# Kernel tuning notes

Measured on AMD Instinct MI355X. Metric: run time of the kernel, lower is better.

The kernel has to match this reference:

```python
import jax, jax.numpy as jnp
import numpy as np

B, N, F, S = 32, 512, 101, 10   # batch, set size, str_fea_len, expansion_size
E, H, L = 128, 4, 3             # embed_dim, num_heads, n_encoders
EH = E * H
TAB = 100                       # atom-feature table rows


def _ln(x, g, b, eps=1e-5):
    m = jnp.mean(x, -1, keepdims=True)
    v = jnp.var(x, -1, keepdims=True)
    return (x - m) / jnp.sqrt(v + eps) * g + b


def setup_inputs() -> dict:
    key = jax.random.key(0)
    ks = iter(jax.random.split(key, 48))
    nrm = lambda shape: jax.random.normal(next(ks), shape, jnp.float32) * 0.05
    return {
        'str_fea': jax.random.uniform(next(ks), (B, N, F), jnp.float32),
        'comp_fea': jax.random.randint(next(ks), (B, N), 0, TAB),
        'cell_fea': jax.random.normal(next(ks), (B, 6), jnp.float32),
        'af_table': jax.random.uniform(next(ks), (TAB, 92), jnp.float32),
        'comp_w': nrm((92, E)), 'comp_b': jnp.zeros((E,), jnp.float32),
        'emb_w': nrm(((F - 1) * S, E)), 'emb_b': jnp.zeros((E,), jnp.float32),
        'ln_g': jnp.ones((L, E), jnp.float32), 'ln_b': jnp.zeros((L, E), jnp.float32),
        'wq': nrm((L, E, EH)), 'bq': jnp.zeros((L, EH), jnp.float32),
        'wk': nrm((L, E, EH)), 'bk': jnp.zeros((L, EH), jnp.float32),
        'wv': nrm((L, E, EH)), 'bv': jnp.zeros((L, EH), jnp.float32),
        'inproj_w': nrm((L, EH, 3 * EH)), 'inproj_b': jnp.zeros((L, 3 * EH), jnp.float32),
        'out_w': nrm((L, EH, E)), 'out_b': jnp.zeros((L, E), jnp.float32),
        'ffn_w': nrm((L, E, E)), 'ffn_b': jnp.zeros((L, E), jnp.float32),
        'ln2_g': jnp.ones((E,), jnp.float32), 'ln2_b': jnp.zeros((E,), jnp.float32),
        'final_w': nrm((E, 1)), 'final_b': jnp.zeros((1,), jnp.float32),
    }


def reference(str_fea, comp_fea, cell_fea, af_table, comp_w, comp_b, emb_w, emb_b,
              ln_g, ln_b, wq, bq, wk, bk, wv, bv, inproj_w, inproj_b,
              out_w, out_b, ffn_w, ffn_b, ln2_g, ln2_b, final_w, final_b):
    weights = str_fea[:, :, 0:1]                                  # [B,N,1]
    # AtomFeaturizer + composition embedding
    comp = af_table[comp_fea] @ comp_w + comp_b                   # [B,N,E]
    # DistanceExpansion: (1 - (d - i/S))**2 for i in 0..S-1
    d = str_fea[:, :, 1:]                                         # [B,N,F-1]
    starter = jnp.arange(S, dtype=str_fea.dtype) / S
    de = (1.0 - (d[..., None] - starter)) ** 2                    # [B,N,F-1,S]
    de = de.reshape(d.shape[0], d.shape[1], (F - 1) * S)
    strf = de @ emb_w + emb_b                                     # [B,N,E]
    x = comp + strf
    x_init = x
    mask = jnp.sum(weights, -1) == 0.0                            # [B,N] key padding
    w_row = weights[..., 0]                                       # [B,N]
    hd = EH // H
    scale = 1.0 / np.sqrt(hd)
    for l in range(L):
        xn = _ln(x, ln_g[l], ln_b[l])
        qin = xn @ wq[l] + bq[l]                                  # [B,N,EH]
        kin = xn @ wk[l] + bk[l]
        vin = xn @ wv[l] + bv[l]                                  # used as V in manual attention
        # torch.nn.MultiheadAttention in-projection (v-block unused: att_output discarded)
        q = qin @ inproj_w[l][:, :EH] + inproj_b[l][:EH]
        k = kin @ inproj_w[l][:, EH:2 * EH] + inproj_b[l][EH:2 * EH]
        qh = q.reshape(q.shape[0], q.shape[1], H, hd)
        kh = k.reshape(k.shape[0], k.shape[1], H, hd)
        logits = jnp.einsum('bihd,bjhd->bhij', qh, kh) * scale    # [B,H,N,N]
        logits = jnp.where(mask[:, None, None, :], -1e9, logits)
        attn = jnp.mean(jax.nn.softmax(logits, -1), axis=1)       # head-averaged [B,N,N]
        # external edge-weight masking + renormalization
        aw = attn * w_row[:, None, :]
        aw = aw / jnp.sum(aw, -1, keepdims=True)
        att_out = jnp.einsum('bij,bjd->bid', aw, vin)             # [B,N,EH]
        o1 = x + att_out @ out_w[l] + out_b[l]
        o2 = jax.nn.softplus(_ln(o1, ln_g[l], ln_b[l]) @ ffn_w[l] + ffn_b[l])
        x = _ln(o1 + o2, ln_g[l], ln_b[l])
    x = jnp.sum(weights * (x + x_init), axis=1)                   # weighted pool [B,E]
    x = _ln(x, ln2_g, ln2_b)
    return x @ final_w + final_b                                  # [B,1]
```

## Files before the change

### kernel.cpp

```cpp
#include <hip/hip_runtime.h>
#include <math.h>

#define B_ 32
#define N_ 512
#define F_ 101
#define E_ 128
#define H_ 4
#define EH_ 512
#define L_ 3
#define M_ (B_*N_)

typedef __attribute__((ext_vector_type(8))) short s8v;
typedef __attribute__((ext_vector_type(8))) unsigned short us8v;
typedef __attribute__((ext_vector_type(4))) float f4v;
typedef __attribute__((ext_vector_type(4))) unsigned int u4v;

__device__ __forceinline__ unsigned short f2bf(float f){
  unsigned int u = __builtin_bit_cast(unsigned int, f);
  u += 0x7fffu + ((u>>16)&1u);
  return (unsigned short)(u>>16);
}
__device__ __forceinline__ float bf2f(unsigned int h){
  unsigned int u = h<<16; return __builtin_bit_cast(float, u);
}
__device__ __forceinline__ float softplus_f(float v) {
  return fmaxf(v, 0.f) + log1pf(__expf(-fabsf(v)));
}

#define GLOAD16(gp, lp) __builtin_amdgcn_global_load_lds( \
    (__attribute__((address_space(1))) unsigned int*)(gp), \
    (__attribute__((address_space(3))) unsigned int*)(lp), 16, 0, 0)

#define MFMA16(a,b,c) __builtin_amdgcn_mfma_f32_16x16x32_bf16(a,b,c,0,0,0)

__global__ __launch_bounds__(256) void prepA_kernel(
    const float* __restrict__ wq, const float* __restrict__ wk,
    const float* __restrict__ bq, const float* __restrict__ bk,
    const float* __restrict__ inproj_w,
    float* __restrict__ effpart, float* __restrict__ bpart) {
  __shared__ float As[64][132];
  __shared__ float Bs[64][68];
  const int blk = blockIdx.x;
  const int t = threadIdx.x;
  if (blk < 384) {
    const int bx = blk % 48, ks = blk / 48;
    const int lq = bx>>3, nt = bx&7;
    const int l = lq>>1, qk = lq&1;
    const int bn = nt*64;
    const int k0 = ks*64;
    const float* A = (qk ? wk : wq) + (size_t)l*128*512;
    const float* IP = inproj_w + (size_t)l*512*1536 + qk*512 + bn;
    float acc[8][4];
    #pragma unroll
    for (int i=0;i<8;++i)
      #pragma unroll
      for (int j=0;j<4;++j) acc[i][j]=0.f;
    const int r0 = (t&15)*8, c0 = (t>>4)*4;
    {
      int r = t & 127, half = t>>7;
      #pragma unroll
      for (int u=0;u<8;++u){
        float4 a = *(const float4*)(A + (size_t)r*512 + k0 + half*32 + u*4);
        int kk = half*32 + u*4;
        As[kk+0][r]=a.x; As[kk+1][r]=a.y; As[kk+2][r]=a.z; As[kk+3][r]=a.w;
      }
      int kk = t>>2, cb = (t&3)*16;
      #pragma unroll
      for (int u=0;u<4;++u)
        *(float4*)&Bs[kk][cb+u*4] = *(const float4*)(IP + (size_t)(k0+kk)*1536 + cb + u*4);
    }
    __syncthreads();
    for (int k2=0;k2<64;++k2){
      float4 b = *(const float4*)&Bs[k2][c0];
      float4 a0 = *(const float4*)&As[k2][r0];
      float4 a1 = *(const float4*)&As[k2][r0+4];
      float av[8] = {a0.x,a0.y,a0.z,a0.w,a1.x,a1.y,a1.z,a1.w};
      #pragma unroll
      for (int i=0;i<8;++i){
        acc[i][0] += av[i]*b.x; acc[i][1] += av[i]*b.y;
        acc[i][2] += av[i]*b.z; acc[i][3] += av[i]*b.w;
      }
    }
    #pragma unroll
    for (int j=0;j<4;++j){
      float* dst = effpart + (((size_t)ks*48 + bx)*64 + c0 + j)*128 + r0;
      float4 v0 = {acc[0][j], acc[1][j], acc[2][j], acc[3][j]};
      float4 v1 = {acc[4][j], acc[5][j], acc[6][j], acc[7][j]};
      *(float4*)dst = v0;
      *(float4*)(dst+4) = v1;
    }
  } else {
    const int idxb = blk - 384;
    const int lq = idxb>>3, kt = idxb&7;
    const int l = lq>>1, qk = lq&1;
    const float* bv = (qk?bk:bq) + l*512 + kt*64;
    const float* IP = inproj_w + ((size_t)l*512 + kt*64)*1536 + qk*512;
    float a0=0.f, a1=0.f;
    for (int kk=0; kk<64; ++kk){
      float b = bv[kk];
      const float* row = IP + (size_t)kk*1536;
      a0 += b*row[t];
      a1 += b*row[t+256];
    }
    bpart[(lq*8+kt)*512 + t]       = a0;
    bpart[(lq*8+kt)*512 + t + 256] = a1;
  }
}

__global__ __launch_bounds__(256) void prepB_kernel(
    const float* __restrict__ effpart, const float* __restrict__ bpart,
    const float* __restrict__ wv, const float* __restrict__ out_w,
    const float* __restrict__ ffn_w,
    const float* __restrict__ inproj_b, const float* __restrict__ bvv,
    const float* __restrict__ emb_w, const float* __restrict__ comp_w,
    const float* __restrict__ str_fea, const int* __restrict__ comp_fea,
    const float* __restrict__ af_table,
    unsigned short* __restrict__ wqkvT, unsigned short* __restrict__ outT,
    unsigned short* __restrict__ ffnT, float* __restrict__ bqkv,
    unsigned short* __restrict__ WHi, unsigned short* __restrict__ WLo,
    float* __restrict__ Cpart,
    unsigned short* __restrict__ FHi, unsigned short* __restrict__ FLo,
    float* __restrict__ w_row) {
  const int blk = blockIdx.x;
  const int t = threadIdx.x;
  if (blk < 1536) {
    int idx = blk*256 + t;
    int m = idx & 127;
    int n = (idx>>7) & 511;
    int lq = idx >> 16;
    int l = lq>>1, qk = lq&1;
    size_t base = (((size_t)(lq*8 + (n>>6)))*64 + (n&63))*128 + m;
    float v = 0.f;
    #pragma unroll
    for (int ks=0;ks<8;++ks) v += effpart[(size_t)ks*393216 + base];
    wqkvT[((size_t)l*1536 + qk*512 + n)*128 + m] = f2bf(v);
  } else if (blk < 1662) {
    const int b2 = blk - 1536;
    if (b2 < 108) {
      __shared__ float tile[64][65];
      const float* src; unsigned short* dst; int srcld, dstld;
      if (b2 < 48) {
        int lay = b2/16, rem = b2%16, kt = rem>>3, nt = rem&7;
        src = wv + ((size_t)lay*128 + kt*64)*512 + nt*64; srcld = 512;
        dst = wqkvT + ((size_t)lay*1536 + 1024 + nt*64)*128 + kt*64; dstld = 128;
      } else if (b2 < 96) {
        int b3 = b2-48; int lay = b3/16, rem = b3%16, kt = rem>>1, nt = rem&1;
        src = out_w + ((size_t)lay*512 + kt*64)*128 + nt*64; srcld = 128;
        dst = outT + ((size_t)lay*128 + nt*64)*512 + kt*64; dstld = 512;
      } else {
        int b4 = b2-96; int lay = b4/4, rem = b4%4, kt = rem>>1, nt = rem&1;
        src = ffn_w + ((size_t)lay*128 + kt*64)*128 + nt*64; srcld = 128;
        dst = ffnT + ((size_t)lay*128 + nt*64)*128 + kt*64; dstld = 128;
      }
      #pragma unroll
      for (int rp=0; rp<4; ++rp){
        int r = rp*16 + (t>>4), c = (t&15)*4;
        float4 v = *(const float4*)(src + (size_t)r*srcld + c);
        tile[r][c+0]=v.x; tile[r][c+1]=v.y; tile[r][c+2]=v.z; tile[r][c+3]=v.w;
      }
      __syncthreads();
      #pragma unroll
      for (int wp=0; wp<2; ++wp){
        int n = wp*32 + (t>>3), kk = (t&7)*8;
        us8v pk;
        #pragma unroll
        for (int e=0;e<8;++e) pk[e] = f2bf(tile[kk+e][n]);
        *(us8v*)(dst + (size_t)n*dstld + kk) = pk;
      }
    } else {
      int idx = (b2-108)*256 + t;
      if (idx < 4608) {
        int l = idx/1536, n = idx - l*1536;
        float v;
        if (n < 1024) {
          int qk = n>>9, c = n&511;
          v = inproj_b[(size_t)l*1536 + n];
          #pragma unroll
          for (int kt=0;kt<8;++kt) v += bpart[((l*2+qk)*8+kt)*512 + c];
        } else {
          v = bvv[(size_t)l*512 + (n-1024)];
        }
        bqkv[idx] = v;
      }
    }
  } else if (blk < 1674) {
    if (t < 128) {
      int p = blk - 1662, e = t;
      if (p < 10) {
        float Cp = 0.f;
        for (int ff=0; ff<10; ++ff){
          int f = p*10+ff;
          float A=0.f, Bv=0.f;
          #pragma unroll
          for (int s=0;s<10;++s){
            float wvv = emb_w[(size_t)(f*10+s)*128 + e];
            A += wvv; Bv += 0.2f*s*wvv; Cp += 0.01f*(s*s)*wvv;
          }
          int kA = 92+f, kB = 192+f;
          unsigned short hA = f2bf(A);
          WHi[e*320+kA]=hA; WLo[e*320+kA]=f2bf(A - bf2f(hA));
          unsigned short hB = f2bf(Bv);
          WHi[e*320+kB]=hB; WLo[e*320+kB]=f2bf(Bv - bf2f(hB));
        }
        Cpart[p*128+e] = Cp;
      } else if (p == 10) {
        for (int kk=0;kk<92;++kk){
          float v = comp_w[(size_t)kk*128 + e];
          unsigned short h = f2bf(v);
          WHi[e*320+kk]=h; WLo[e*320+kk]=f2bf(v - bf2f(h));
        }
      } else {
        for (int kk=292;kk<320;++kk){ WHi[e*320+kk]=0; WLo[e*320+kk]=0; }
      }
    }
  } else {
    int g = (blk-1674)*256 + t;
    int row = g / 40, seg = g - row*40;
    const float* sr = str_fea + (size_t)row*F_;
    if (seg == 0) w_row[row] = sr[0];
    const float* af = af_table + (size_t)comp_fea[row]*92;
    const int c0 = seg*8;
    us8v hi, lo;
    #pragma unroll
    for (int e=0;e<8;++e){
      int kk = c0+e; float v;
      if (kk < 92) v = af[kk];
      else if (kk < 192) { float u = 1.f - sr[1+kk-92]; v = u*u; }
      else if (kk < 292) v = 1.f - sr[1+kk-192];
      else v = 0.f;
      unsigned short h = f2bf(v);
      hi[e] = h; lo[e] = f2bf(v - bf2f(h));
    }
    *(us8v*)(FHi + (size_t)row*320 + c0) = hi;
    *(us8v*)(FLo + (size_t)row*320 + c0) = lo;
  }
}

__global__ __launch_bounds__(256) void embgemm_kernel(
    const unsigned short* __restrict__ FHi, const unsigned short* __restrict__ FLo,
    const unsigned short* __restrict__ WHi, const unsigned short* __restrict__ WLo,
    const float* __restrict__ Cpart, const float* __restrict__ comp_b,
    const float* __restrict__ emb_b,
    const float* __restrict__ g0, const float* __restrict__ b0,
    float* __restrict__ x, float* __restrict__ x_init,
    unsigned short* __restrict__ xnb) {
  __shared__ unsigned short lds[24576];
  unsigned short* AHi = lds;
  unsigned short* ALo = lds + 4096;
  unsigned short* BHi = lds + 8192;
  unsigned short* BLo = lds + 16384;
  const int bm = blockIdx.x*64;
  const int t = threadIdx.x, w = t>>6, l = t&63;
  f4v acc[8];
  #pragma unroll
  for (int i=0;i<8;++i) acc[i] = (f4v){0.f,0.f,0.f,0.f};
  const int srow = t>>3, sseg = t&7;
  for (int k0=0;k0<320;k0+=64){
    #pragma unroll
    for (int c=0;c<2;++c){
      int row = c*32+srow;
      GLOAD16(FHi + (size_t)(bm+row)*320 + k0 + ((sseg^(row&7))<<3), (char*)AHi + c*4096 + w*1024);
      GLOAD16(FLo + (size_t)(bm+row)*320 + k0 + ((sseg^(row&7))<<3), (char*)ALo + c*4096 + w*1024);
    }
    #pragma unroll
    for (int c=0;c<4;++c){
      int row = c*32+srow;
      GLOAD16(WHi + (size_t)row*320 + k0 + ((sseg^(row&7))<<3), (char*)BHi + c*4096 + w*1024);
      GLOAD16(WLo + (size_t)row*320 + k0 + ((sseg^(row&7))<<3), (char*)BLo + c*4096 + w*1024);
    }
    __syncthreads();
    #pragma unroll
    for (int ks=0;ks<2;++ks){
      int arow = w*16 + (l&15);
      int aswz = ((((l>>4)+ks*4) ^ (arow&7))<<4);
      s8v ah = *(const s8v*)((const char*)AHi + arow*128 + aswz);
      s8v al = *(const s8v*)((const char*)ALo + arow*128 + aswz);
      #pragma unroll
      for (int ct=0;ct<8;++ct){
        int col = ct*16 + (l&15);
        int bswz = ((((l>>4)+ks*4) ^ (col&7))<<4);
        s8v bh = *(const s8v*)((const char*)BHi + col*128 + bswz);
        s8v bl = *(const s8v*)((const char*)BLo + col*128 + bswz);
        acc[ct] = MFMA16(ah, bh, acc[ct]);
        acc[ct] = MFMA16(ah, bl, acc[ct]);
        acc[ct] = MFMA16(al, bh, acc[ct]);
      }
    }
    __syncthreads();
  }
  float vv[8][4], gc[8], bc[8];
  #pragma unroll
  for (int ct=0;ct<8;++ct){
    int c = ct*16 + (l&15);
    float be = comp_b[c] + emb_b[c];
    for (int p=0;p<10;++p) be += Cpart[p*128+c];
    gc[ct] = g0[c]; bc[ct] = b0[c];
    #pragma unroll
    for (int r=0;r<4;++r) vv[ct][r] = acc[ct][r] + be;
  }
  #pragma unroll
  for (int r=0;r<4;++r){
    float s=0.f, sq=0.f;
    #pragma unroll
    for (int ct=0;ct<8;++ct){ s += vv[ct][r]; sq += vv[ct][r]*vv[ct][r]; }
    #pragma unroll
    for (int m=1;m<16;m<<=1){ s += __shfl_xor(s,m,64); sq += __shfl_xor(sq,m,64); }
    float mean = s*(1.f/128.f);
    float rstd = rsqrtf(sq*(1.f/128.f) - mean*mean + 1e-5f);
    int row = bm + w*16 + (l>>4)*4 + r;
    #pragma unroll
    for (int ct=0;ct<8;++ct){
      int c = ct*16 + (l&15);
      float v = vv[ct][r];
      x[(size_t)row*128 + c] = v;
      x_init[(size_t)row*128 + c] = v;
      xnb[(size_t)row*128 + c] = f2bf((v-mean)*rstd*gc[ct] + bc[ct]);
    }
  }
}

template<int RT>
__global__ __launch_bounds__(256) void mgemm_kernel(
    const unsigned short* __restrict__ A,
    const unsigned short* __restrict__ Bt,
    const float* __restrict__ bias,
    unsigned short* __restrict__ Cb,
    unsigned short* __restrict__ vT,
    int K) {
  constexpr int BM = RT*32;
  __shared__ float smem[8192];
  unsigned short* Al = (unsigned short*)smem;
  unsigned short* Bl = Al + BM*64;
  const int bm = blockIdx.x*BM;
  const int bn = blockIdx.y*128;
  const int t = threadIdx.x;
  const int w = t>>6, l = t&63;
  const int wr = w>>1, wc = w&1;
  f4v acc[RT][4];
  #pragma unroll
  for (int i=0;i<RT;++i)
    #pragma unroll
    for (int j=0;j<4;++j) acc[i][j] = (f4v){0.f,0.f,0.f,0.f};
  const int srow = t>>3, sseg = t&7;
  for (int k0 = 0; k0 < K; k0 += 64) {
    #pragma unroll
    for (int c=0;c<BM/32;++c){
      int row = c*32 + srow;
      GLOAD16(A + (size_t)(bm+row)*K + k0 + ((sseg ^ (row&7))<<3),
              (char*)Al + c*4096 + w*1024);
    }
    #pragma unroll
    for (int c=0;c<4;++c){
      int row = c*32 + srow;
      GLOAD16(Bt + (size_t)(bn+row)*K + k0 + ((sseg ^ (row&7))<<3),
              (char*)Bl + c*4096 + w*1024);
    }
    __syncthreads();
    #pragma unroll
    for (int ks=0;ks<2;++ks){
      s8v bf[4];
      #pragma unroll
      for (int ct=0;ct<4;++ct){
        int col = wc*64 + ct*16 + (l&15);
        bf[ct] = *(const s8v*)((const char*)Bl + col*128 + ((((l>>4)+ks*4) ^ (col&7))<<4));
      }
      #pragma unroll
      for (int rt=0;rt<RT;++rt){
        int arow = wr*(RT*16) + rt*16 + (l&15);
        s8v af = *(const s8v*)((const char*)Al + arow*128 + ((((l>>4)+ks*4) ^ (arow&7))<<4));
        #pragma unroll
        for (int ct=0;ct<4;++ct)
          acc[rt][ct] = MFMA16(af, bf[ct], acc[rt][ct]);
      }
    }
    __syncthreads();
  }
  float bia[4];
  #pragma unroll
  for (int ct=0;ct<4;++ct) bia[ct] = bias[bn + wc*64 + ct*16 + (l&15)];
  unsigned short* lds16 = (unsigned short*)smem;
  if (bn < 1024) {
    #pragma unroll
    for (int rt=0;rt<RT;++rt)
      #pragma unroll
      for (int ct=0;ct<4;++ct)
        #pragma unroll
        for (int r=0;r<4;++r){
          int rr = wr*(RT*16) + rt*16 + (l>>4)*4 + r;
          int cc = wc*64 + ct*16 + (l&15);
          lds16[rr*128 + cc] = f2bf(acc[rt][ct][r] + bia[ct]);
        }
    __syncthreads();
    #pragma unroll
    for (int it=0; it<BM/16; ++it){
      int row = it*16 + (t>>4), seg = t&15;
      u4v v = *(const u4v*)(lds16 + row*128 + seg*8);
      *(u4v*)(Cb + (size_t)(bm+row)*1024 + bn + seg*8) = v;
    }
  } else {
    #pragma unroll
    for (int rt=0;rt<RT;++rt)
      #pragma unroll
      for (int ct=0;ct<4;++ct){
        int rbase = bm + wr*(RT*16) + rt*16 + (l>>4)*4;
        int bb = rbase >> 9, nn = rbase & 511;
        int d = bn - 1024 + wc*64 + ct*16 + (l&15);
        unsigned int lo = (unsigned int)f2bf(acc[rt][ct][0] + bia[ct])
                        | ((unsigned int)f2bf(acc[rt][ct][1] + bia[ct])<<16);
        unsigned int hi = (unsigned int)f2bf(acc[rt][ct][2] + bia[ct])
                        | ((unsigned int)f2bf(acc[rt][ct][3] + bia[ct])<<16);
        uint2 pk; pk.x = lo; pk.y = hi;
        *(uint2*)(vT + ((size_t)(bb*512 + d))*512 + nn) = pk;
      }
  }
}

#define STG_KH(dst, hh, j0s) { \
  _Pragma("unroll") \
  for (int c_=0;c_<8;++c_){ \
    int row_ = c_*32 + w*4 + (l>>4); \
    GLOAD16(qkb + (size_t)(b*512 + (j0s) + row_)*1024 + 512 + (hh)*128 + (((l&15) ^ (row_&7))<<3), \
            (dst) + c_*8192 + w*1024); } }

#define STG_VT(dst, j0s) { \
  _Pragma("unroll") \
  for (int c_=0;c_<4;++c_){ \
    int d_ = c_*128 + w*16 + (l>>2); \
    GLOAD16(vT + ((size_t)(b*512 + d_))*512 + (j0s) + (((l&3) ^ ((d_>>1)&3))<<3), \
            (dst) + c_*8192 + w*1024); } }

#define STG_B1(dst, k0s) { \
  _Pragma("unroll") \
  for (int c_=0;c_<2;++c_){ \
    int n_ = c_*64 + w*8 + (l>>3); \
    GLOAD16(outTl + (size_t)n_*512 + (k0s) + (((l&7) ^ (n_&7))<<3), \
            (dst) + (c_*64 + w*8)*128); } }

#define STG_F1() { \
  _Pragma("unroll") \
  for (int c2_=0;c2_<4;++c2_){ \
    int kh_ = c2_>>1, c_ = c2_&1; \
    int n_ = c_*64 + w*8 + (l>>3); \
    GLOAD16(ffnTl + (size_t)n_*128 + kh_*64 + (((l&7) ^ (n_&7))<<3), \
            ffnB + kh_*16384 + (c_*64 + w*8)*128); } }

__global__ __launch_bounds__(512, 2) void attnU_kernel(
    const unsigned short* __restrict__ qkb, const unsigned short* __restrict__ vT,
    const float* __restrict__ w_row,
    const unsigned short* __restrict__ outTl, const float* __restrict__ out_b,
    const unsigned short* __restrict__ ffnTl, const float* __restrict__ ffn_b,
    float* __restrict__ x, unsigned short* __restrict__ xnb,
    const float* __restrict__ g1, const float* __restrict__ b1,
    const float* __restrict__ g2, const float* __restrict__ b2) {
  __shared__ char smem[136704];
  char* const Kt0 = smem;
  char* const Kt1 = smem + 65536;
  char* const cALc = smem;
  unsigned short* const cAL = (unsigned short*)smem;
  char* const VbA = smem + 66560;
  char* const VbB = smem + 99328;
  float* const w_s    = (float*)(smem + 132096);
  float* const Spart  = (float*)(smem + 134144);
  float* const Rpart  = (float*)(smem + 134656);
  float* const sinv_l = (float*)(smem + 135168);
  float* const rho_l  = (float*)(smem + 135424);
  float* const zinv_l = (float*)(smem + 136448);
  unsigned short* const outL = (unsigned short*)smem;
  char* const BtA = smem + 66560;
  char* const BtB = smem + 82944;
  float* const vst = (float*)(smem + 99328);
  char* const xnl  = smem;
  char* const ffnB = smem + 16384;

  const int id = blockIdx.x;
  const int b  = (id & 7) | ((id >> 6) << 3);
  const int i0 = ((id >> 3) & 7) * 64;
  const int bm = b*512 + i0;
  const int t = threadIdx.x, w = t>>6, l = t&63;
  const int wi = w & 3, wd = w >> 2;
  const int ib = wi*16 + (l>>4)*4;
  const int arow = wi*16 + (l&15);
  const float SC2 = 1.4426950408889634f * 0.088388347648318447f;

  for (int j=t; j<512; j+=512) w_s[j] = w_row[b*512+j];

  float c_[2][8][4];
  #pragma unroll
  for (int tt=0;tt<2;++tt)
    #pragma unroll
    for (int js=0;js<8;++js)
      #pragma unroll
      for (int r=0;r<4;++r) c_[tt][js][r] = 0.f;

  STG_KH(Kt0, 0, 0);
  __syncthreads();

  char* Kc = Kt0; char* Kn = Kt1;
  #pragma unroll 1
  for (int h=0; h<4; ++h){
    s8v qf[4];
    {
      const unsigned short* qbase = qkb + ((size_t)(bm + arow))*1024 + h*128;
      #pragma unroll
      for (int ks=0;ks<4;++ks) qf[ks] = *(const s8v*)(qbase + ks*32 + (l>>4)*8);
    }
    float Ex[2][8][4];
    #pragma unroll
    for (int tt=0; tt<2; ++tt){
      if (tt==0) { STG_KH(Kn, h, 256); }
      else if (h<3) { STG_KH(Kn, h+1, 0); }
      #pragma unroll
      for (int jsub=0;jsub<8;++jsub){
        const int jcol = wd*128 + jsub*16 + (l&15);
        f4v a = (f4v){0.f,0.f,0.f,0.f};
        #pragma unroll
        for (int ks=0;ks<4;++ks){
          int g = ks*4 + (l>>4);
          s8v kf = *(const s8v*)(Kc + jcol*256 + ((g ^ (jcol&7))<<4));
          a = MFMA16(qf[ks], kf, a);
        }
        #pragma unroll
        for (int r=0;r<4;++r) Ex[tt][jsub][r] = exp2f(a[r]*SC2);
      }
      __syncthreads();
      char* tmp = Kc; Kc = Kn; Kn = tmp;
    }
    float sp[4] = {0.f,0.f,0.f,0.f};
    float rp[4] = {0.f,0.f,0.f,0.f};
    #pragma unroll
    for (int tt=0;tt<2;++tt)
      #pragma unroll
      for (int jsub=0;jsub<8;++jsub){
        int jg = tt*256 + wd*128 + jsub*16 + (l&15);
        float wv = w_s[jg];
        float mw = (wv != 0.f) ? 1.f : 0.f;
        #pragma unroll
        for (int r=0;r<4;++r){
          sp[r] += Ex[tt][jsub][r]*mw;
          rp[r] += Ex[tt][jsub][r]*wv;
        }
      }
    #pragma unroll
    for (int r=0;r<4;++r){
      float s = sp[r], rv = rp[r];
      s += __shfl_xor(s,1,64); rv += __shfl_xor(rv,1,64);
      s += __shfl_xor(s,2,64); rv += __shfl_xor(rv,2,64);
      s += __shfl_xor(s,4,64); rv += __shfl_xor(rv,4,64);
      s += __shfl_xor(s,8,64); rv += __shfl_xor(rv,8,64);
      sp[r] = s; rp[r] = rv;
    }
    if ((l&15)==0){
      #pragma unroll
      for (int r=0;r<4;++r){
        Spart[wd*64 + ib + r] = sp[r];
        Rpart[wd*64 + ib + r] = rp[r];
      }
    }
    __syncthreads();
    if (t < 64){
      float S = Spart[t] + Spart[64+t];
      float R = Rpart[t] + Rpart[64+t];
      float si = 1.f/S;
      sinv_l[t] = si;
      rho_l[h*64+t] = R*si;
    }
    __syncthreads();
    float siv[4];
    #pragma unroll
    for (int r=0;r<4;++r) siv[r] = sinv_l[ib + r];
    #pragma unroll
    for (int tt=0;tt<2;++tt)
      #pragma unroll
      for (int jsub=0;jsub<8;++jsub)
        #pragma unroll
        for (int r=0;r<4;++r)
          c_[tt][jsub][r] += Ex[tt][jsub][r]*siv[r];
  }

  STG_VT(VbA, 0);
  if (t < 64)
    zinv_l[t] = 1.f/(rho_l[t] + rho_l[64+t] + rho_l[128+t] + rho_l[192+t]);
  #pragma unroll
  for (int tt=0;tt<2;++tt)
    #pragma unroll
    for (int jsub=0;jsub<8;++jsub){
      int jg = tt*256 + wd*128 + jsub*16 + (l&15);
      float wv = w_s[jg];
      #pragma unroll
      for (int r=0;r<4;++r)
        cAL[(ib+r)*520 + jg] = f2bf(c_[tt][jsub][r]*wv);
    }
  __syncthreads();
  float zv[4];
  #pragma unroll
  for (int r=0;r<4;++r) zv[r] = zinv_l[ib + r];

  f4v pacc[16];
  #pragma unroll
  for (int ct=0;ct<16;++ct) pacc[ct] = (f4v){0.f,0.f,0.f,0.f};
  {
    char* Vc = VbA; char* Vn = VbB;
    #pragma unroll 1
    for (int vt=0; vt<16; ++vt){
      if (vt < 15) STG_VT(Vn, (vt+1)*32);
      int kidx = l>>4;
      s8v af = *(const s8v*)(cALc + arow*1040 + vt*64 + (kidx<<4));
      #pragma unroll
      for (int ct=0;ct<16;++ct){
        int d = wd*256 + ct*16 + (l&15);
        s8v vf = *(const s8v*)(Vc + d*64 + ((kidx ^ ((d>>1)&3))<<4));
        pacc[ct] = MFMA16(af, vf, pacc[ct]);
      }
      __syncthreads();
      char* tmp = Vc; Vc = Vn; Vn = tmp;
    }
  }

  #pragma unroll
  for (int ct=0;ct<16;++ct){
    int d = wd*256 + ct*16 + (l&15);
    #pragma unroll
    for (int r=0;r<4;++r)
      outL[(ib+r)*520 + d] = f2bf(pacc[ct][r]*zv[r]);
  }
  STG_B1(BtA, 0);
  __syncthreads();

  f4v acc1[4];
  #pragma unroll
  for (int ct=0;ct<4;++ct) acc1[ct] = (f4v){0.f,0.f,0.f,0.f};
  {
    char* Bc = BtA; char* Bn = BtB;
    #pragma unroll 1
    for (int tt=0; tt<8; ++tt){
      if (tt < 7) STG_B1(Bn, (tt+1)*64);
      #pragma unroll
      for (int ks=0;ks<2;++ks){
        int kidx = (l>>4) + ks*4;
        s8v af = *(const s8v*)((const char*)outL + arow*1040 + tt*128 + (kidx<<4));
        #pragma unroll
        for (int ct=0;ct<4;++ct){
          int n = wd*64 + ct*16 + (l&15);
          s8v bf = *(const s8v*)(Bc + n*128 + ((kidx ^ (n&7))<<4));
          acc1[ct] = MFMA16(af, bf, acc1[ct]);
        }
      }
      __syncthreads();
      char* tmp = Bc; Bc = Bn; Bn = tmp;
    }
  }

  #pragma unroll
  for (int ct=0;ct<4;++ct){
    int cc = wd*64 + ct*16 + (l&15);
    float ob = out_b[cc];
    #pragma unroll
    for (int r=0;r<4;++r){
      int rr = wi*16 + (l>>4)*4 + r;
      vst[rr*128 + cc] = acc1[ct][r] + ob + x[(size_t)(bm+rr)*128 + cc];
    }
  }
  STG_F1();
  __syncthreads();

  {
    const float2 g1v = *(const float2*)(g1 + l*2);
    const float2 b1v = *(const float2*)(b1 + l*2);
    #pragma unroll
    for (int rr=0; rr<8; ++rr){
      int row = w*8 + rr;
      float2 vv = *(const float2*)&vst[row*128 + l*2];
      float s = vv.x+vv.y, sq = vv.x*vv.x + vv.y*vv.y;
      #pragma unroll
      for (int m=1;m<64;m<<=1){ s += __shfl_xor(s,m,64); sq += __shfl_xor(sq,m,64); }
      float mean = s*(1.f/128.f);
      float rstd = rsqrtf(sq*(1.f/128.f) - mean*mean + 1e-5f);
      float xa = (vv.x-mean)*rstd*g1v.x + b1v.x;
      float xb = (vv.y-mean)*rstd*g1v.y + b1v.y;
      int col = l*2;
      int byte = row*256 + (((col>>3) ^ (row&7))<<4) + ((col&7)<<1);
      unsigned int pk = (unsigned int)f2bf(xa) | ((unsigned int)f2bf(xb)<<16);
      *(unsigned int*)(xnl + byte) = pk;
    }
  }
  __syncthreads();

  f4v acc2[4];
  #pragma unroll
  for (int ct=0;ct<4;++ct) acc2[ct] = (f4v){0.f,0.f,0.f,0.f};
  #pragma unroll
  for (int ks2=0;ks2<4;++ks2){
    int kidx2 = (l>>4) + ks2*4;
    s8v af = *(const s8v*)(xnl + arow*256 + ((kidx2 ^ (arow&7))<<4));
    int kh = ks2>>1, ksb = ks2&1;
    int kb = (l>>4) + ksb*4;
    #pragma unroll
    for (int ct=0;ct<4;++ct){
      int n = wd*64 + ct*16 + (l&15);
      s8v bf = *(const s8v*)(ffnB + kh*16384 + n*128 + ((kb ^ (n&7))<<4));
      acc2[ct] = MFMA16(af, bf, acc2[ct]);
    }
  }
  #pragma unroll
  for (int ct=0;ct<4;++ct){
    int cc = wd*64 + ct*16 + (l&15);
    float fb = ffn_b[cc];
    #pragma unroll
    for (int r=0;r<4;++r){
      int rr = wi*16 + (l>>4)*4 + r;
      vst[rr*128 + cc] += softplus_f(acc2[ct][r] + fb);
    }
  }
  __syncthreads();

  {
    const float2 g1v = *(const float2*)(g1 + l*2);
    const float2 b1v = *(const float2*)(b1 + l*2);
    #pragma unroll
    for (int rr=0; rr<8; ++rr){
      int row = w*8 + rr;
      float2 vv = *(const float2*)&vst[row*128 + l*2];
      float s = vv.x+vv.y, sq = vv.x*vv.x + vv.y*vv.y;
      #pragma unroll
      for (int m=1;m<64;m<<=1){ s += __shfl_xor(s,m,64); sq += __shfl_xor(sq,m,64); }
      float mean = s*(1.f/128.f);
      float rstd = rsqrtf(sq*(1.f/128.f) - mean*mean + 1e-5f);
      float xa = (vv.x-mean)*rstd*g1v.x + b1v.x;
      float xb = (vv.y-mean)*rstd*g1v.y + b1v.y;
      float2 xo; xo.x = xa; xo.y = xb;
      *(float2*)(x + (size_t)(bm+row)*128 + l*2) = xo;
      if (g2) {
        float s2 = xa+xb, sq2 = xa*xa + xb*xb;
        #pragma unroll
        for (int m=1;m<64;m<<=1){ s2 += __shfl_xor(s2,m,64); sq2 += __shfl_xor(sq2,m,64); }
        float mean2 = s2*(1.f/128.f);
        float rstd2 = rsqrtf(sq2*(1.f/128.f) - mean2*mean2 + 1e-5f);
        const float2 g2v = *(const float2*)(g2 + l*2);
        const float2 b2v = *(const float2*)(b2 + l*2);
        float ya = (xa-mean2)*rstd2*g2v.x + b2v.x;
        float yb = (xb-mean2)*rstd2*g2v.y + b2v.y;
        unsigned int pk = (unsigned int)f2bf(ya) | ((unsigned int)f2bf(yb)<<16);
        *(unsigned int*)(xnb + (size_t)(bm+row)*128 + l*2) = pk;
      }
    }
  }
}

__global__ __launch_bounds__(256) void poolfinal_kernel(
    const float* __restrict__ x, const float* __restrict__ x_init,
    const float* __restrict__ w_row,
    const float* __restrict__ g, const float* __restrict__ bt,
    const float* __restrict__ fw, const float* __restrict__ fb,
    float* __restrict__ out) {
  __shared__ float red[2][128];
  __shared__ float red2[4];
  __shared__ float red3[2];
  const int b = blockIdx.x;
  const int t = threadIdx.x;
  const int e = t & 127, half = t >> 7;
  float acc = 0.f;
  for (int n = half*256; n < half*256+256; ++n) {
    float w = w_row[(size_t)b*N_ + n];
    size_t o = ((size_t)b*N_ + n)*E_ + e;
    acc += w * (x[o] + x_init[o]);
  }
  red[half][e] = acc;
  __syncthreads();
  float s=0.f, sq=0.f, v=0.f;
  if (t < 128) {
    v = red[0][t] + red[1][t];
    s = v; sq = v*v;
    #pragma unroll
    for (int m = 1; m < 64; m <<= 1) { s += __shfl_xor(s, m, 64); sq += __shfl_xor(sq, m, 64); }
    if ((t&63) == 0) { red2[(t>>6)*2] = s; red2[(t>>6)*2+1] = sq; }
  }
  __syncthreads();
  float p = 0.f;
  if (t < 128) {
    s = red2[0] + red2[2]; sq = red2[1] + red2[3];
    float mean = s*(1.f/E_), var = sq*(1.f/E_) - mean*mean;
    float rstd = rsqrtf(var + 1e-5f);
    float xl = (v - mean)*rstd*g[t] + bt[t];
    p = xl * fw[t];
    #pragma unroll
    for (int m = 1; m < 64; m <<= 1) p += __shfl_xor(p, m, 64);
    if ((t&63) == 0) red3[t>>6] = p;
  }
  __syncthreads();
  if (t == 0) out[b] = red3[0] + red3[1] + fb[0];
}

extern "C" void kernel_launch(void* const* d_in, const int* in_sizes, int n_in,
                              void* d_out, int out_size, void* d_ws, size_t ws_size,
                              hipStream_t stream) {
  (void)in_sizes; (void)n_in; (void)out_size; (void)ws_size;
  const float* str_fea  = (const float*)d_in[0];
  const int*   comp_fea = (const int*)  d_in[1];
  const float* af_table = (const float*)d_in[3];
  const float* comp_w   = (const float*)d_in[4];
  const float* comp_b   = (const float*)d_in[5];
  const float* emb_w    = (const float*)d_in[6];
  const float* emb_b    = (const float*)d_in[7];
  const float* ln_g     = (const float*)d_in[8];
  const float* ln_b     = (const float*)d_in[9];
  const float* wq       = (const float*)d_in[10];
  const float* bq       = (const float*)d_in[11];
  const float* wk       = (const float*)d_in[12];
  const float* bk       = (const float*)d_in[13];
  const float* wv       = (const float*)d_in[14];
  const float* bv       = (const float*)d_in[15];
  const float* inproj_w = (const float*)d_in[16];
  const float* inproj_b = (const float*)d_in[17];
  const float* out_w    = (const float*)d_in[18];
  const float* out_b    = (const float*)d_in[19];
  const float* ffn_w    = (const float*)d_in[20];
  const float* ffn_b    = (const float*)d_in[21];
  const float* ln2_g    = (const float*)d_in[22];
  const float* ln2_b    = (const float*)d_in[23];
  const float* final_w  = (const float*)d_in[24];
  const float* final_b  = (const float*)d_in[25];
  float* out = (float*)d_out;

  float* ws = (float*)d_ws;
  size_t off = 0;
  float* x      = ws + off; off += 2097152;
  float* x_init = ws + off; off += 2097152;
  float* w_row  = ws + off; off += 16384;
  unsigned short* xnb  = (unsigned short*)(ws + off); off += 1048576;
  unsigned short* qkb  = (unsigned short*)(ws + off); off += 8388608;
  unsigned short* vTb  = (unsigned short*)(ws + off); off += 4194304;
  float* bpart  = ws + off; off += 24576;
  float* effpart= ws + off; off += 3145728;
  float* bqkv   = ws + off; off += 4608;
  unsigned short* wqkvT = (unsigned short*)(ws + off); off += 294912;
  unsigned short* outT  = (unsigned short*)(ws + off); off += 98304;
  unsigned short* ffnT  = (unsigned short*)(ws + off); off += 24576;
  unsigned short* FHi   = (unsigned short*)(ws + off); off += 2621440;
  unsigned short* FLo   = (unsigned short*)(ws + off); off += 2621440;
  unsigned short* WHi   = (unsigned short*)(ws + off); off += 20480;
  unsigned short* WLo   = (unsigned short*)(ws + off); off += 20480;
  float* Cpart  = ws + off; off += 1280;

  prepA_kernel<<<432, 256, 0, stream>>>(wq, wk, bq, bk, inproj_w, effpart, bpart);
  prepB_kernel<<<4234, 256, 0, stream>>>(effpart, bpart, wv, out_w, ffn_w,
                                         inproj_b, bv, emb_w, comp_w,
                                         str_fea, comp_fea, af_table,
                                         wqkvT, outT, ffnT, bqkv,
                                         WHi, WLo, Cpart, FHi, FLo, w_row);
  embgemm_kernel<<<M_/64, 256, 0, stream>>>(FHi, FLo, WHi, WLo, Cpart, comp_b, emb_b,
                                            ln_g, ln_b, x, x_init, xnb);

  for (int l = 0; l < L_; ++l) {
    mgemm_kernel<4><<<dim3(M_/128, 12), 256, 0, stream>>>(
        xnb, wqkvT + (size_t)l*196608, bqkv + l*1536, qkb, vTb, 128);
    attnU_kernel<<<256, 512, 0, stream>>>(
        qkb, vTb, w_row,
        outT + (size_t)l*65536, out_b + (size_t)l*E_,
        ffnT + (size_t)l*16384, ffn_b + (size_t)l*E_,
        x, xnb, ln_g + l*E_, ln_b + l*E_,
        (l < 2) ? (ln_g + (l+1)*E_) : nullptr,
        (l < 2) ? (ln_b + (l+1)*E_) : nullptr);
  }

  poolfinal_kernel<<<B_, 256, 0, stream>>>(x, x_init, w_row, ln2_g, ln2_b,
                                           final_w, final_b, out);
}
```

Measured before the change: 304.3 us.

## Remap attention warp tiling so each warp covers all 64 rows

Changes the per-warp work split in the attention kernel: each of the 8 warps now computes all four 16-row groups against a narrower slice of key columns (32 instead of 128) and value dims (64 instead of 256). Each K or V fragment read from shared memory then feeds four MFMAs instead of one, which cuts LDS traffic per MFMA. In exchange every warp must load four Q fragments and four A fragments, and the row-sum reduction now spans 8 partial buffers, which needs more shared memory. Register pressure also shifts under the 2-blocks-per-SM launch bound.

```diff
diff --git a/kernel.cpp b/kernel.cpp
--- a/kernel.cpp
+++ b/kernel.cpp
@@ -444,7 +444,7 @@
     GLOAD16(ffnTl + (size_t)n_*128 + kh_*64 + (((l&7) ^ (n_&7))<<3), \
             ffnB + kh_*16384 + (c_*64 + w*8)*128); } }
 
-__global__ __launch_bounds__(512, 2) void attnU_kernel(
+__global__ __launch_bounds__(512, 2) void attnV_kernel(
     const unsigned short* __restrict__ qkb, const unsigned short* __restrict__ vT,
     const float* __restrict__ w_row,
     const unsigned short* __restrict__ outTl, const float* __restrict__ out_b,
@@ -452,7 +452,7 @@
     float* __restrict__ x, unsigned short* __restrict__ xnb,
     const float* __restrict__ g1, const float* __restrict__ b1,
     const float* __restrict__ g2, const float* __restrict__ b2) {
-  __shared__ char smem[136704];
+  __shared__ char smem[139776];
   char* const Kt0 = smem;
   char* const Kt1 = smem + 65536;
   char* const cALc = smem;
@@ -461,10 +461,10 @@
   char* const VbB = smem + 99328;
   float* const w_s    = (float*)(smem + 132096);
   float* const Spart  = (float*)(smem + 134144);
-  float* const Rpart  = (float*)(smem + 134656);
-  float* const sinv_l = (float*)(smem + 135168);
-  float* const rho_l  = (float*)(smem + 135424);
-  float* const zinv_l = (float*)(smem + 136448);
+  float* const Rpart  = (float*)(smem + 136192);
+  float* const sinv_l = (float*)(smem + 138240);
+  float* const rho_l  = (float*)(smem + 138496);
+  float* const zinv_l = (float*)(smem + 139520);
   unsigned short* const outL = (unsigned short*)smem;
   char* const BtA = smem + 66560;
   char* const BtB = smem + 82944;
@@ -478,19 +478,20 @@
   const int bm = b*512 + i0;
   const int t = threadIdx.x, w = t>>6, l = t&63;
   const int wi = w & 3, wd = w >> 2;
-  const int ib = wi*16 + (l>>4)*4;
   const int arow = wi*16 + (l&15);
   const float SC2 = 1.4426950408889634f * 0.088388347648318447f;
 
   for (int j=t; j<512; j+=512) w_s[j] = w_row[b*512+j];
 
-  float c_[2][8][4];
+  float c_[2][4][2][4];
   #pragma unroll
   for (int tt=0;tt<2;++tt)
     #pragma unroll
-    for (int js=0;js<8;++js)
-      #pragma unroll
-      for (int r=0;r<4;++r) c_[tt][js][r] = 0.f;
+    for (int ig=0;ig<4;++ig)
+      #pragma unroll
+      for (int js=0;js<2;++js)
+        #pragma unroll
+        for (int r=0;r<4;++r) c_[tt][ig][js][r] = 0.f;
 
   STG_KH(Kt0, 0, 0);
   __syncthreads();
@@ -498,83 +499,105 @@
   char* Kc = Kt0; char* Kn = Kt1;
   #pragma unroll 1
   for (int h=0; h<4; ++h){
-    s8v qf[4];
-    {
-      const unsigned short* qbase = qkb + ((size_t)(bm + arow))*1024 + h*128;
-      #pragma unroll
-      for (int ks=0;ks<4;++ks) qf[ks] = *(const s8v*)(qbase + ks*32 + (l>>4)*8);
-    }
-    float Ex[2][8][4];
+    s8v qf[4][4];
+    #pragma unroll
+    for (int ig=0; ig<4; ++ig){
+      const unsigned short* qbase = qkb + ((size_t)(bm + ig*16 + (l&15)))*1024 + h*128;
+      #pragma unroll
+      for (int ks=0;ks<4;++ks) qf[ig][ks] = *(const s8v*)(qbase + ks*32 + (l>>4)*8);
+    }
+    float Ex[2][4][2][4];
     #pragma unroll
     for (int tt=0; tt<2; ++tt){
       if (tt==0) { STG_KH(Kn, h, 256); }
       else if (h<3) { STG_KH(Kn, h+1, 0); }
       #pragma unroll
-      for (int jsub=0;jsub<8;++jsub){
-        const int jcol = wd*128 + jsub*16 + (l&15);
-        f4v a = (f4v){0.f,0.f,0.f,0.f};
+      for (int jsub=0;jsub<2;++jsub){
+        const int jcol = w*32 + jsub*16 + (l&15);
+        f4v a[4];
+        #pragma unroll
+        for (int ig=0;ig<4;++ig) a[ig] = (f4v){0.f,0.f,0.f,0.f};
         #pragma unroll
         for (int ks=0;ks<4;++ks){
           int g = ks*4 + (l>>4);
           s8v kf = *(const s8v*)(Kc + jcol*256 + ((g ^ (jcol&7))<<4));
-          a = MFMA16(qf[ks], kf, a);
+          #pragma unroll
+          for (int ig=0;ig<4;++ig)
+            a[ig] = MFMA16(qf[ig][ks], kf, a[ig]);
         }
         #pragma unroll
-        for (int r=0;r<4;++r) Ex[tt][jsub][r] = exp2f(a[r]*SC2);
+        for (int ig=0;ig<4;++ig)
+          #pragma unroll
+          for (int r=0;r<4;++r) Ex[tt][ig][jsub][r] = exp2f(a[ig][r]*SC2);
       }
       __syncthreads();
       char* tmp = Kc; Kc = Kn; Kn = tmp;
     }
-    float sp[4] = {0.f,0.f,0.f,0.f};
-    float rp[4] = {0.f,0.f,0.f,0.f};
+    float sp[4][4], rp[4][4];
+    #pragma unroll
+    for (int ig=0;ig<4;++ig)
+      #pragma unroll
+      for (int r=0;r<4;++r){ sp[ig][r]=0.f; rp[ig][r]=0.f; }
     #pragma unroll
     for (int tt=0;tt<2;++tt)
       #pragma unroll
-      for (int jsub=0;jsub<8;++jsub){
-        int jg = tt*256 + wd*128 + jsub*16 + (l&15);
+      for (int jsub=0;jsub<2;++jsub){
+        int jg = tt*256 + w*32 + jsub*16 + (l&15);
         float wv = w_s[jg];
         float mw = (wv != 0.f) ? 1.f : 0.f;
         #pragma unroll
+        for (int ig=0;ig<4;++ig)
+          #pragma unroll
+          for (int r=0;r<4;++r){
+            sp[ig][r] += Ex[tt][ig][jsub][r]*mw;
+            rp[ig][r] += Ex[tt][ig][jsub][r]*wv;
+          }
+      }
+    #pragma unroll
+    for (int ig=0;ig<4;++ig)
+      #pragma unroll
+      for (int r=0;r<4;++r){
+        float s = sp[ig][r], rv = rp[ig][r];
+        s += __shfl_xor(s,1,64); rv += __shfl_xor(rv,1,64);
+        s += __shfl_xor(s,2,64); rv += __shfl_xor(rv,2,64);
+        s += __shfl_xor(s,4,64); rv += __shfl_xor(rv,4,64);
+        s += __shfl_xor(s,8,64); rv += __shfl_xor(rv,8,64);
+        sp[ig][r] = s; rp[ig][r] = rv;
+      }
+    if ((l&15)==0){
+      #pragma unroll
+      for (int ig=0;ig<4;++ig)
+        #pragma unroll
         for (int r=0;r<4;++r){
-          sp[r] += Ex[tt][jsub][r]*mw;
-          rp[r] += Ex[tt][jsub][r]*wv;
+          int i = ig*16 + (l>>4)*4 + r;
+          Spart[w*64 + i] = sp[ig][r];
+          Rpart[w*64 + i] = rp[ig][r];
         }
-      }
-    #pragma unroll
-    for (int r=0;r<4;++r){
-      float s = sp[r], rv = rp[r];
-      s += __shfl_xor(s,1,64); rv += __shfl_xor(rv,1,64);
-      s += __shfl_xor(s,2,64); rv += __shfl_xor(rv,2,64);
-      s += __shfl_xor(s,4,64); rv += __shfl_xor(rv,4,64);
-      s += __shfl_xor(s,8,64); rv += __shfl_xor(rv,8,64);
-      sp[r] = s; rp[r] = rv;
-    }
-    if ((l&15)==0){
-      #pragma unroll
-      for (int r=0;r<4;++r){
-        Spart[wd*64 + ib + r] = sp[r];
-        Rpart[wd*64 + ib + r] = rp[r];
-      }
     }
     __syncthreads();
     if (t < 64){
-      float S = Spart[t] + Spart[64+t];
-      float R = Rpart[t] + Rpart[64+t];
+      float S = 0.f, R = 0.f;
+      #pragma unroll
+      for (int ww=0;ww<8;++ww){ S += Spart[ww*64+t]; R += Rpart[ww*64+t]; }
       float si = 1.f/S;
       sinv_l[t] = si;
       rho_l[h*64+t] = R*si;
     }
     __syncthreads();
-    float siv[4];
-    #pragma unroll
-    for (int r=0;r<4;++r) siv[r] = sinv_l[ib + r];
+    float siv[4][4];
+    #pragma unroll
+    for (int ig=0;ig<4;++ig)
+      #pragma unroll
+      for (int r=0;r<4;++r) siv[ig][r] = sinv_l[ig*16 + (l>>4)*4 + r];
     #pragma unroll
     for (int tt=0;tt<2;++tt)
       #pragma unroll
-      for (int jsub=0;jsub<8;++jsub)
-        #pragma unroll
-        for (int r=0;r<4;++r)
-          c_[tt][jsub][r] += Ex[tt][jsub][r]*siv[r];
+      for (int ig=0;ig<4;++ig)
+        #pragma unroll
+        for (int jsub=0;jsub<2;++jsub)
+          #pragma unroll
+          for (int r=0;r<4;++r)
+            c_[tt][ig][jsub][r] += Ex[tt][ig][jsub][r]*siv[ig][r];
   }
 
   STG_VT(VbA, 0);
@@ -583,33 +606,44 @@
   #pragma unroll
   for (int tt=0;tt<2;++tt)
     #pragma unroll
-    for (int jsub=0;jsub<8;++jsub){
-      int jg = tt*256 + wd*128 + jsub*16 + (l&15);
-      float wv = w_s[jg];
-      #pragma unroll
-      for (int r=0;r<4;++r)
-        cAL[(ib+r)*520 + jg] = f2bf(c_[tt][jsub][r]*wv);
-    }
+    for (int ig=0;ig<4;++ig)
+      #pragma unroll
+      for (int jsub=0;jsub<2;++jsub){
+        int jg = tt*256 + w*32 + jsub*16 + (l&15);
+        float wv = w_s[jg];
+        #pragma unroll
+        for (int r=0;r<4;++r)
+          cAL[(ig*16 + (l>>4)*4 + r)*520 + jg] = f2bf(c_[tt][ig][jsub][r]*wv);
+      }
   __syncthreads();
-  float zv[4];
-  #pragma unroll
-  for (int r=0;r<4;++r) zv[r] = zinv_l[ib + r];
-
-  f4v pacc[16];
-  #pragma unroll
-  for (int ct=0;ct<16;++ct) pacc[ct] = (f4v){0.f,0.f,0.f,0.f};
+  float zv[4][4];
+  #pragma unroll
+  for (int ig=0;ig<4;++ig)
+    #pragma unroll
+    for (int r=0;r<4;++r) zv[ig][r] = zinv_l[ig*16 + (l>>4)*4 + r];
+
+  f4v pacc[4][4];
+  #pragma unroll
+  for (int ig=0;ig<4;++ig)
+    #pragma unroll
+    for (int ds=0;ds<4;++ds) pacc[ig][ds] = (f4v){0.f,0.f,0.f,0.f};
   {
     char* Vc = VbA; char* Vn = VbB;
     #pragma unroll 1
     for (int vt=0; vt<16; ++vt){
       if (vt < 15) STG_VT(Vn, (vt+1)*32);
       int kidx = l>>4;
-      s8v af = *(const s8v*)(cALc + arow*1040 + vt*64 + (kidx<<4));
-      #pragma unroll
-      for (int ct=0;ct<16;++ct){
-        int d = wd*256 + ct*16 + (l&15);
+      s8v af[4];
+      #pragma unroll
+      for (int ig=0;ig<4;++ig)
+        af[ig] = *(const s8v*)(cALc + (ig*16 + (l&15))*1040 + vt*64 + (kidx<<4));
+      #pragma unroll
+      for (int dsub=0;dsub<4;++dsub){
+        int d = w*64 + dsub*16 + (l&15);
         s8v vf = *(const s8v*)(Vc + d*64 + ((kidx ^ ((d>>1)&3))<<4));
-        pacc[ct] = MFMA16(af, vf, pacc[ct]);
+        #pragma unroll
+        for (int ig=0;ig<4;++ig)
+          pacc[ig][dsub] = MFMA16(af[ig], vf, pacc[ig][dsub]);
       }
       __syncthreads();
       char* tmp = Vc; Vc = Vn; Vn = tmp;
@@ -617,12 +651,14 @@
   }
 
   #pragma unroll
-  for (int ct=0;ct<16;++ct){
-    int d = wd*256 + ct*16 + (l&15);
-    #pragma unroll
-    for (int r=0;r<4;++r)
-      outL[(ib+r)*520 + d] = f2bf(pacc[ct][r]*zv[r]);
-  }
+  for (int ig=0;ig<4;++ig)
+    #pragma unroll
+    for (int dsub=0;dsub<4;++dsub){
+      int d = w*64 + dsub*16 + (l&15);
+      #pragma unroll
+      for (int r=0;r<4;++r)
+        outL[(ig*16 + (l>>4)*4 + r)*520 + d] = f2bf(pacc[ig][dsub][r]*zv[ig][r]);
+    }
   STG_B1(BtA, 0);
   __syncthreads();
 
@@ -853,7 +889,7 @@
   for (int l = 0; l < L_; ++l) {
     mgemm_kernel<4><<<dim3(M_/128, 12), 256, 0, stream>>>(
         xnb, wqkvT + (size_t)l*196608, bqkv + l*1536, qkb, vTb, 128);
-    attnU_kernel<<<256, 512, 0, stream>>>(
+    attnV_kernel<<<256, 512, 0, stream>>>(
         qkb, vTb, w_row,
         outT + (size_t)l*65536, out_b + (size_t)l*E_,
         ffnT + (size_t)l*16384, ffn_b + (size_t)l*E_,
```

Result: slower. 389.0 us (+27.8%).
